# Kernel tuning notes

Measured on AMD Instinct MI355X. Metric: run time of the kernel, lower is better.

The kernel has to match this reference:

```python
import jax, jax.numpy as jnp
import numpy as np

IMG_SIZE = 1280
NUM_ANCHORS = 3
NUM_CLASSES = 80
B, G = 16, 160
C = NUM_ANCHORS * (6 + NUM_CLASSES)  # 258


def setup_inputs() -> dict:
    key = jax.random.key(0)
    k1, k2, k3 = jax.random.split(key, 3)
    x = jax.random.normal(k1, (B, C, G, G), dtype=jnp.float32)
    target = jax.random.uniform(k2, (B, 50, 7), dtype=jnp.float32)
    # anchor box priors in pixels (positive sizes)
    anchors = jax.random.uniform(k3, (NUM_ANCHORS, 2), dtype=jnp.float32) * 60.0 + 4.0
    return {"x": x, "target": target, "anchors": anchors}


def reference(x, target, anchors):
    # x: [B, A*Cp, G, G] -> [B, A, G, G, Cp]
    Bb, Cc, Gg, _ = x.shape
    A = anchors.shape[0]
    Cp = Cc // A
    y = x.reshape(Bb, A, Cp, Gg, Gg).transpose(0, 1, 3, 4, 2)

    off_x = jax.nn.sigmoid(y[..., 0])          # [B,A,G,G]
    off_y = jax.nn.sigmoid(y[..., 1])
    scale_w = jnp.exp(y[..., 2])
    scale_h = jnp.exp(y[..., 3])
    anchor_yaw = y[..., 4]
    anchor_conf = jax.nn.sigmoid(y[..., 5])
    anchor_cls = jnp.argmax(y[..., 6:], axis=-1).astype(x.dtype)

    stride = IMG_SIZE / Gg
    grid = jnp.arange(Gg, dtype=x.dtype)
    grid_x = grid[None, :]   # broadcasts over rows (repeat((G,1)))
    grid_y = grid[:, None]   # its transpose

    anchor_x = jnp.floor((off_x + grid_x) * stride)
    anchor_y = jnp.floor((off_y + grid_y) * stride)
    anchor_w = scale_w * anchors[:, 0][None, :, None, None]
    anchor_h = scale_h * anchors[:, 1][None, :, None, None]

    # [B, A, G, G, 7] -> [B, A*G*G, 7]
    pred = jnp.stack(
        [anchor_x, anchor_y, anchor_w, anchor_h, anchor_yaw, anchor_conf, anchor_cls],
        axis=-1,
    ).reshape(Bb, A * Gg * Gg, 7)
    return pred
```

## Files before the change

kernel.cpp:

```cpp
#include <hip/hip_runtime.h>

namespace {

constexpr int Gg     = 160;
constexpr int NA     = 3;
constexpr int NB     = 16;
constexpr int CP     = 86;
constexpr int NCLS   = 80;
constexpr int PLANE  = Gg * Gg;
constexpr int QPP    = PLANE / 4;
constexpr int TOTAL  = NB * NA * QPP;
constexpr float STRIDE = 8.0f;

union F4 { float4 v; float f[4]; };

__device__ __forceinline__ float4 ld4(const float* p) {
    return *reinterpret_cast<const float4*>(p);
}

__device__ __forceinline__ float fsigmoid(float v) {
    return __builtin_amdgcn_rcpf(1.0f + __expf(-v));
}

__global__ __launch_bounds__(256) void anchor_decode(
    const float* __restrict__ x,
    const float* __restrict__ anchors,
    float* __restrict__ out)
{
    const int t = blockIdx.x * 256 + threadIdx.x;
    if (t >= TOTAL) return;

    const int q   = t % QPP;
    const int ba  = t / QPP;
    const int a   = ba % NA;
    const int pix = q * 4;
    const int i   = pix / Gg;
    const int j   = pix - i * Gg;

    const float* xp = x + (size_t)ba * CP * PLANE + pix;

    F4 c0, c1, c2, c3, c4, c5;
    c0.v = ld4(xp + 0 * PLANE);
    c1.v = ld4(xp + 1 * PLANE);
    c2.v = ld4(xp + 2 * PLANE);
    c3.v = ld4(xp + 3 * PLANE);
    c4.v = ld4(xp + 4 * PLANE);
    c5.v = ld4(xp + 5 * PLANE);

    F4 best; best.v = ld4(xp + 6 * PLANE);
    float bidx[4] = {0.f, 0.f, 0.f, 0.f};
    #pragma unroll 8
    for (int c = 1; c < NCLS; ++c) {
        F4 u; u.v = ld4(xp + (size_t)(6 + c) * PLANE);
        #pragma unroll
        for (int p = 0; p < 4; ++p) {
            const bool gt = u.f[p] > best.f[p];
            best.f[p] = gt ? u.f[p] : best.f[p];
            bidx[p]   = gt ? (float)c : bidx[p];
        }
    }

    const float aw = anchors[a * 2 + 0];
    const float ah = anchors[a * 2 + 1];
    const float fi = (float)i;
    const float fj = (float)j;

    alignas(16) float fout[28];
    #pragma unroll
    for (int p = 0; p < 4; ++p) {
        fout[p * 7 + 0] = floorf((fsigmoid(c0.f[p]) + (fj + (float)p)) * STRIDE);
        fout[p * 7 + 1] = floorf((fsigmoid(c1.f[p]) + fi) * STRIDE);
        fout[p * 7 + 2] = __expf(c2.f[p]) * aw;
        fout[p * 7 + 3] = __expf(c3.f[p]) * ah;
        fout[p * 7 + 4] = c4.f[p];
        fout[p * 7 + 5] = fsigmoid(c5.f[p]);
        fout[p * 7 + 6] = bidx[p];
    }

    float* op = out + (size_t)(ba * PLANE + pix) * 7;
    #pragma unroll
    for (int k = 0; k < 7; ++k) {
        *reinterpret_cast<float4*>(op + k * 4) =
            *reinterpret_cast<float4*>(&fout[k * 4]);
    }
}

}

extern "C" void kernel_launch(void* const* d_in, const int* in_sizes, int n_in,
                              void* d_out, int out_size, void* d_ws, size_t ws_size,
                              hipStream_t stream) {
    const float* x       = (const float*)d_in[0];
    const float* anchors = (const float*)d_in[2];
    float* out           = (float*)d_out;

    const int blocks = (TOTAL + 255) / 256;
    anchor_decode<<<blocks, 256, 0, stream>>>(x, anchors, out);
}
```

Baseline: 561.7 us.

## Stage output through LDS for coalesced stores and use nontemporal loads

Each thread now writes its 28 output floats to a padded LDS row. After a barrier, each wave reads them back transposed so that consecutive lanes store consecutive float4s, making global writes fully coalesced. Input loads and output stores use nontemporal hints, class loads are batched eight at a time, and launch bounds request higher occupancy. In exchange the kernel adds LDS traffic and a block barrier, and the bounds check is removed, which relies on the total thread count being an exact multiple of the block size.

New measurement: 528.1 us. 1.06x faster.

```diff
diff --git a/kernel.cpp b/kernel.cpp
--- a/kernel.cpp
+++ b/kernel.cpp
@@ -11,77 +11,103 @@
 constexpr int QPP    = PLANE / 4;
 constexpr int TOTAL  = NB * NA * QPP;
 constexpr float STRIDE = 8.0f;
+constexpr int LROW   = 29;
 
-union F4 { float4 v; float f[4]; };
+typedef float f4 __attribute__((ext_vector_type(4)));
 
-__device__ __forceinline__ float4 ld4(const float* p) {
-    return *reinterpret_cast<const float4*>(p);
+union F4 { f4 v; float f[4]; };
+
+__device__ __forceinline__ f4 ldnt(const float* p) {
+    return __builtin_nontemporal_load(reinterpret_cast<const f4*>(p));
 }
 
 __device__ __forceinline__ float fsigmoid(float v) {
     return __builtin_amdgcn_rcpf(1.0f + __expf(-v));
 }
 
-__global__ __launch_bounds__(256) void anchor_decode(
+__global__ __launch_bounds__(256, 6) void anchor_decode(
     const float* __restrict__ x,
     const float* __restrict__ anchors,
     float* __restrict__ out)
 {
-    const int t = blockIdx.x * 256 + threadIdx.x;
-    if (t >= TOTAL) return;
+    __shared__ float lds[256 * LROW];
+
+    const int t    = blockIdx.x * 256 + threadIdx.x;
+    const int lane = threadIdx.x & 63;
 
     const int q   = t % QPP;
     const int ba  = t / QPP;
-    const int a   = ba % NA;
+    const int a   = ba - (ba / NA) * NA;
     const int pix = q * 4;
     const int i   = pix / Gg;
     const int j   = pix - i * Gg;
 
-    const float* xp = x + (size_t)ba * CP * PLANE + pix;
+    const float* xp = x + (size_t)ba * (CP * PLANE) + pix;
+    const float* cp = xp + (size_t)6 * PLANE;
 
-    F4 c0, c1, c2, c3, c4, c5;
-    c0.v = ld4(xp + 0 * PLANE);
-    c1.v = ld4(xp + 1 * PLANE);
-    c2.v = ld4(xp + 2 * PLANE);
-    c3.v = ld4(xp + 3 * PLANE);
-    c4.v = ld4(xp + 4 * PLANE);
-    c5.v = ld4(xp + 5 * PLANE);
+    float bval[4], bidx[4];
+    #pragma unroll
+    for (int p = 0; p < 4; ++p) { bval[p] = -__builtin_inff(); bidx[p] = 0.0f; }
 
-    F4 best; best.v = ld4(xp + 6 * PLANE);
-    float bidx[4] = {0.f, 0.f, 0.f, 0.f};
-    #pragma unroll 8
-    for (int c = 1; c < NCLS; ++c) {
-        F4 u; u.v = ld4(xp + (size_t)(6 + c) * PLANE);
+    for (int c0 = 0; c0 < NCLS; c0 += 8) {
+        F4 u[8];
         #pragma unroll
-        for (int p = 0; p < 4; ++p) {
-            const bool gt = u.f[p] > best.f[p];
-            best.f[p] = gt ? u.f[p] : best.f[p];
-            bidx[p]   = gt ? (float)c : bidx[p];
+        for (int k = 0; k < 8; ++k)
+            u[k].v = ldnt(cp + (size_t)(c0 + k) * PLANE);
+        #pragma unroll
+        for (int k = 0; k < 8; ++k) {
+            const float fc = (float)(c0 + k);
+            #pragma unroll
+            for (int p = 0; p < 4; ++p) {
+                const bool gt = u[k].f[p] > bval[p];
+                bval[p] = gt ? u[k].f[p] : bval[p];
+                bidx[p] = gt ? fc : bidx[p];
+            }
         }
     }
+
+    F4 h0, h1, h2, h3, h4, h5;
+    h0.v = ldnt(xp + 0 * PLANE);
+    h1.v = ldnt(xp + 1 * PLANE);
+    h2.v = ldnt(xp + 2 * PLANE);
+    h3.v = ldnt(xp + 3 * PLANE);
+    h4.v = ldnt(xp + 4 * PLANE);
+    h5.v = ldnt(xp + 5 * PLANE);
 
     const float aw = anchors[a * 2 + 0];
     const float ah = anchors[a * 2 + 1];
     const float fi = (float)i;
     const float fj = (float)j;
 
-    alignas(16) float fout[28];
+    float* lrow = lds + (size_t)threadIdx.x * LROW;
     #pragma unroll
     for (int p = 0; p < 4; ++p) {
-        fout[p * 7 + 0] = floorf((fsigmoid(c0.f[p]) + (fj + (float)p)) * STRIDE);
-        fout[p * 7 + 1] = floorf((fsigmoid(c1.f[p]) + fi) * STRIDE);
-        fout[p * 7 + 2] = __expf(c2.f[p]) * aw;
-        fout[p * 7 + 3] = __expf(c3.f[p]) * ah;
-        fout[p * 7 + 4] = c4.f[p];
-        fout[p * 7 + 5] = fsigmoid(c5.f[p]);
-        fout[p * 7 + 6] = bidx[p];
+        lrow[p * 7 + 0] = floorf((fsigmoid(h0.f[p]) + (fj + (float)p)) * STRIDE);
+        lrow[p * 7 + 1] = floorf((fsigmoid(h1.f[p]) + fi) * STRIDE);
+        lrow[p * 7 + 2] = __expf(h2.f[p]) * aw;
+        lrow[p * 7 + 3] = __expf(h3.f[p]) * ah;
+        lrow[p * 7 + 4] = h4.f[p];
+        lrow[p * 7 + 5] = fsigmoid(h5.f[p]);
+        lrow[p * 7 + 6] = bidx[p];
     }
 
-    float* op = out + (size_t)(ba * PLANE + pix) * 7;
+    __syncthreads();
+
+    const int wv = threadIdx.x >> 6;
+    const float* wbase = lds + (size_t)wv * 64 * LROW;
+    const int q0 = q - lane;
+    float* op = out + ((size_t)ba * PLANE + (size_t)q0 * 4) * 7;
+
     #pragma unroll
     for (int k = 0; k < 7; ++k) {
-        *reinterpret_cast<float4*>(op + k * 4) =
-            *reinterpret_cast<float4*>(&fout[k * 4]);
+        F4 w;
+        #pragma unroll
+        for (int e = 0; e < 4; ++e) {
+            const int f = k * 256 + lane * 4 + e;
+            w.f[e] = wbase[(f / 28) * LROW + (f % 28)];
+        }
+        __builtin_nontemporal_store(
+            w.v, reinterpret_cast<f4*>(op + k * 256 + lane * 4));
     }
 }
 
```
